# Kernel tuning notes

Measured on AMD Instinct MI355X. Metric: run time of the kernel, lower is better.

The kernel has to match this reference:

```python
import jax, jax.numpy as jnp
import numpy as np

HID, FFN, NE, TOPK = 1024, 4096, 8, 2


def setup_inputs() -> dict:
    key = jax.random.key(0)
    ks = jax.random.split(key, 4)
    x = jax.random.normal(ks[0], (2, 2048, HID), dtype=jnp.float32)
    # router: nn.Linear(hidden, num_experts, bias=False), init std=0.02; stored as [H, E]
    Wr = jax.random.normal(ks[1], (HID, NE), dtype=jnp.float32) * 0.02
    # per-expert FFN weights stacked on leading expert axis
    W1 = jax.random.normal(ks[2], (NE, HID, FFN), dtype=jnp.float32) * (1.0 / np.sqrt(HID))
    b1 = jnp.zeros((NE, FFN), dtype=jnp.float32)
    W2 = jax.random.normal(ks[3], (NE, FFN, HID), dtype=jnp.float32) * (1.0 / np.sqrt(FFN))
    b2 = jnp.zeros((NE, HID), dtype=jnp.float32)
    return {"x": x, "Wr": Wr, "W1": W1, "b1": b1, "W2": W2, "b2": b2}


def reference(x, Wr, W1, b1, W2, b2):
    B, S, H = x.shape
    E = Wr.shape[1]
    T = B * S
    xf = x.reshape(T, H)                                  # [T, H]
    logits = xf @ Wr                                      # [T, E]
    probs = jax.nn.softmax(logits, axis=-1)
    topk_p, topk_i = jax.lax.top_k(probs, TOPK)           # [T, K]
    topk_p = topk_p / jnp.sum(topk_p, axis=-1, keepdims=True)
    # dense combine weights: c[t, e] = normalized prob if expert e selected for token t else 0
    c = jnp.zeros((T, E), dtype=xf.dtype).at[jnp.arange(T)[:, None], topk_i].add(topk_p)

    def expert_step(acc, ew):
        w1, bb1, w2, bb2, ce = ew                         # ce: [T]
        h = jax.nn.gelu(xf @ w1 + bb1, approximate=False)  # exact GELU like nn.GELU()
        y = h @ w2 + bb2                                  # [T, H]
        return acc + ce[:, None] * y, None

    out, _ = jax.lax.scan(expert_step, jnp.zeros_like(xf), (W1, b1, W2, b2, c.T))
    return out.reshape(B, S, H)
```

## Files before the change

### kernel.cpp

```cpp
#include <hip/hip_runtime.h>
#include <hip/hip_bf16.h>

#define H 1024
#define F 4096
#define NE 8
#define T 4096

typedef unsigned short u16;
typedef float floatx4 __attribute__((ext_vector_type(4)));
typedef short short8 __attribute__((ext_vector_type(8)));

__device__ __forceinline__ u16 f2bf(float f) {
  union { float f; unsigned int u; } c; c.f = f;
  unsigned int u = c.u;
  return (u16)((u + 0x7fffu + ((u >> 16) & 1u)) >> 16);
}

__device__ __forceinline__ void load16_lds(const u16* g, u16* l) {
  __builtin_amdgcn_global_load_lds(
      (const __attribute__((address_space(1))) unsigned int*)g,
      (__attribute__((address_space(3))) unsigned int*)l, 16, 0, 0);
}

__device__ __forceinline__ float gelu_f(float v) {
  float y = fabsf(v) * 0.70710678118f;
  float t = __builtin_amdgcn_rcpf(fmaf(0.3275911f, y, 1.0f));
  float p = t * fmaf(t, fmaf(t, fmaf(t, fmaf(t, 1.061405429f, -1.453152027f),
                                     1.421413741f), -0.284496736f), 0.254829592f);
  float e = __builtin_amdgcn_exp2f(-y * y * 1.44269504f);
  float erfv = fmaf(-p, e, 1.0f);
  return fmaf(0.5f * fabsf(v), erfv, 0.5f * v);
}

__global__ __launch_bounds__(256) void router_kernel(
    const float* __restrict__ x, const float* __restrict__ Wr,
    int* __restrict__ cnt, int* __restrict__ tok, float* __restrict__ wgt) {
  int t = (blockIdx.x * 256 + threadIdx.x) >> 6;
  int lane = threadIdx.x & 63;
  const float* xr = x + (size_t)t * H;
  double p[NE];
#pragma unroll
  for (int e = 0; e < NE; ++e) p[e] = 0.0;
  for (int k = lane; k < H; k += 64) {
    float xv = xr[k];
    const float4* wr4 = reinterpret_cast<const float4*>(Wr + k * NE);
    float4 a = wr4[0], b = wr4[1];
    p[0] += (double)xv * a.x; p[1] += (double)xv * a.y;
    p[2] += (double)xv * a.z; p[3] += (double)xv * a.w;
    p[4] += (double)xv * b.x; p[5] += (double)xv * b.y;
    p[6] += (double)xv * b.z; p[7] += (double)xv * b.w;
  }
#pragma unroll
  for (int e = 0; e < NE; ++e) {
#pragma unroll
    for (int off = 32; off; off >>= 1) p[e] += __shfl_down(p[e], off, 64);
  }
  if (lane == 0) {
    int i0 = 0;
#pragma unroll
    for (int e = 1; e < NE; ++e) if (p[e] > p[i0]) i0 = e;
    int i1 = (i0 == 0) ? 1 : 0;
#pragma unroll
    for (int e = 0; e < NE; ++e) if (e != i0 && p[e] > p[i1]) i1 = e;
    double d = exp(p[i1] - p[i0]);
    float w0 = (float)(1.0 / (1.0 + d));
    float w1 = (float)(d / (1.0 + d));
    int pos0 = atomicAdd(&cnt[i0], 1);
    tok[i0 * T + pos0] = t;
    wgt[i0 * T + pos0] = w0;
    int pos1 = atomicAdd(&cnt[i1], 1);
    tok[i1 * T + pos1] = t | 4096;
    wgt[i1 * T + pos1] = w1;
  }
}

__global__ void offsets_kernel(const int* __restrict__ cnt, int* __restrict__ off) {
  if (threadIdx.x == 0) {
    int s = 0;
#pragma unroll
    for (int e = 0; e < NE; ++e) { off[e] = s; s += cnt[e]; }
    off[NE] = s;
  }
}

__global__ __launch_bounds__(256) void convert_x_kernel(
    const float* __restrict__ x, u16* __restrict__ xb) {
  int i = blockIdx.x * 256 + threadIdx.x;
  float4 v = reinterpret_cast<const float4*>(x)[i];
  ushort4 o;
  o.x = f2bf(v.x); o.y = f2bf(v.y); o.z = f2bf(v.z); o.w = f2bf(v.w);
  reinterpret_cast<ushort4*>(xb)[i] = o;
}

__global__ __launch_bounds__(256) void transpose_both_kernel(
    const float* __restrict__ W1, const float* __restrict__ W2,
    u16* __restrict__ W1t, u16* __restrict__ W2t) {
  __shared__ u16 tile[64][76];
  int z = blockIdx.z;
  int e = z & 7;
  const float* s; u16* d; int R, C, c0, r0;
  if (z < NE) {
    s = W1 + (size_t)e * H * F; d = W1t + (size_t)e * H * F;
    R = H; C = F; c0 = blockIdx.x << 6; r0 = blockIdx.y << 6;
  } else {
    s = W2 + (size_t)e * F * H; d = W2t + (size_t)e * F * H;
    R = F; C = H; c0 = blockIdx.y << 6; r0 = blockIdx.x << 6;
  }
  int t = threadIdx.x;
  int rl = t >> 4, cl = (t & 15) << 2;
#pragma unroll
  for (int i = 0; i < 4; ++i) {
    float4 v = *reinterpret_cast<const float4*>(&s[(size_t)(r0 + rl + i * 16) * C + c0 + cl]);
    ushort4 o; o.x = f2bf(v.x); o.y = f2bf(v.y); o.z = f2bf(v.z); o.w = f2bf(v.w);
    *reinterpret_cast<ushort4*>(&tile[rl + i * 16][cl]) = o;
  }
  __syncthreads();
  int cw = t >> 3, rw = (t & 7) << 3;
#pragma unroll
  for (int i = 0; i < 2; ++i) {
    int c = cw + i * 32;
    short8 o;
#pragma unroll
    for (int j = 0; j < 8; ++j) o[j] = (short)tile[rw + j][c];
    *reinterpret_cast<short8*>(&d[(size_t)(c0 + c) * R + r0 + rw]) = o;
  }
}

__global__ __launch_bounds__(256) void gemm1_kernel(
    const u16* __restrict__ Xb, const u16* __restrict__ W1t,
    const float* __restrict__ b1, const int* __restrict__ cnt,
    const int* __restrict__ off, const int* __restrict__ tok,
    u16* __restrict__ Hc) {
  int e = blockIdx.z;
  int n = cnt[e];
  int m0 = blockIdx.y << 7;
  if (m0 >= n) return;
  int n0 = blockIdx.x << 7;
  int rb = off[e];

  __shared__ alignas(16) u16 As[2][128 * 32];
  __shared__ alignas(16) u16 Bs[2][128 * 32];
  __shared__ int tokS[128];

  int tid = threadIdx.x;
  if (tid < 128) {
    int s = m0 + tid;
    tokS[tid] = (s < n) ? (tok[e * T + s] & 4095) : 0;
  }
  __syncthreads();

  int kchunk = (((tid & 3) ^ ((tid >> 3) & 3))) * 8;
  const u16* W1e = W1t + (size_t)e * F * H;
  const u16* aP0 = Xb + (size_t)tokS[tid >> 2] * H + kchunk;
  const u16* aP1 = Xb + (size_t)tokS[64 + (tid >> 2)] * H + kchunk;
  const u16* bP0 = W1e + (size_t)(n0 + (tid >> 2)) * H + kchunk;
  const u16* bP1 = W1e + (size_t)(n0 + 64 + (tid >> 2)) * H + kchunk;

  int wv = tid >> 6, lane = tid & 63;
  int wm = wv >> 1, wn = wv & 1;
  int quad = lane >> 4, l16 = lane & 15;

  floatx4 acc[4][4];
#pragma unroll
  for (int mt = 0; mt < 4; ++mt)
#pragma unroll
    for (int nt = 0; nt < 4; ++nt) acc[mt][nt] = floatx4{0.f, 0.f, 0.f, 0.f};

  int qa = (quad ^ ((l16 >> 1) & 3)) * 8;
  int aOff[4], bOff[4];
#pragma unroll
  for (int i = 0; i < 4; ++i) {
    aOff[i] = (wm * 64 + i * 16 + l16) * 32 + qa;
    bOff[i] = (wn * 64 + i * 16 + l16) * 32 + qa;
  }

#define STAGE1(buf, kk)                                   \
  do {                                                    \
    load16_lds(aP0 + (kk), &As[buf][tid * 8]);            \
    load16_lds(aP1 + (kk), &As[buf][(tid + 256) * 8]);    \
    load16_lds(bP0 + (kk), &Bs[buf][tid * 8]);            \
    load16_lds(bP1 + (kk), &Bs[buf][(tid + 256) * 8]);    \
  } while (0)

  const int NIT = H / 32;
  STAGE1(0, 0);
  STAGE1(1, 32);
  for (int it = 0; it < NIT; ++it) {
    if (it >= NIT - 1) asm volatile("s_waitcnt vmcnt(0)" ::: "memory");
    else               asm volatile("s_waitcnt vmcnt(4)" ::: "memory");
    __builtin_amdgcn_s_barrier();
    int cur = it & 1;
    short8 av[4], bv[4];
#pragma unroll
    for (int i = 0; i < 4; ++i) {
      av[i] = *reinterpret_cast<const short8*>(&As[cur][aOff[i]]);
      bv[i] = *reinterpret_cast<const short8*>(&Bs[cur][bOff[i]]);
    }
#pragma unroll
    for (int mt = 0; mt < 4; ++mt)
#pragma unroll
      for (int nt = 0; nt < 4; ++nt)
        acc[mt][nt] = __builtin_amdgcn_mfma_f32_16x16x32_bf16(av[mt], bv[nt], acc[mt][nt], 0, 0, 0);
    __builtin_amdgcn_s_barrier();
    if (it + 2 < NIT) STAGE1(cur, (it + 2) * 32);
  }
#undef STAGE1

  float b1v[4];
#pragma unroll
  for (int nt = 0; nt < 4; ++nt)
    b1v[nt] = b1[e * F + n0 + wn * 64 + nt * 16 + l16];
#pragma unroll
  for (int mt = 0; mt < 4; ++mt) {
#pragma unroll
    for (int i = 0; i < 4; ++i) {
      int row = wm * 64 + mt * 16 + quad * 4 + i;
      int gr = m0 + row;
      if (gr < n) {
        u16* hrow = Hc + (size_t)(rb + gr) * F + n0 + wn * 64 + l16;
#pragma unroll
        for (int nt = 0; nt < 4; ++nt) {
          float v = acc[mt][nt][i] + b1v[nt];
          hrow[nt * 16] = f2bf(gelu_f(v));
        }
      }
    }
  }
}

__global__ __launch_bounds__(256) void gemm2_kernel(
    const u16* __restrict__ Hc, const u16* __restrict__ W2t,
    const float* __restrict__ b2, const int* __restrict__ cnt,
    const int* __restrict__ off, const int* __restrict__ tok,
    const float* __restrict__ wgt, float* __restrict__ Yb) {
  int bid = blockIdx.x;
  int e = bid & 7;
  int rem = bid >> 3;
  int by = rem & 31;
  int bx = rem >> 5;
  int n = cnt[e];
  int m0 = by << 7;
  if (m0 >= n) return;
  int n0 = bx << 7;
  int rb = off[e];

  __shared__ alignas(16) u16 As[2][128 * 32];
  __shared__ alignas(16) u16 Bs[2][128 * 32];

  int tid = threadIdx.x;
  int kchunk = (((tid & 3) ^ ((tid >> 3) & 3))) * 8;
  const u16* W2e = W2t + (size_t)e * F * H;
  const u16* aP0 = Hc + (size_t)(rb + m0 + (tid >> 2)) * F + kchunk;
  const u16* aP1 = Hc + (size_t)(rb + m0 + 64 + (tid >> 2)) * F + kchunk;
  const u16* bP0 = W2e + (size_t)(n0 + (tid >> 2)) * F + kchunk;
  const u16* bP1 = W2e + (size_t)(n0 + 64 + (tid >> 2)) * F + kchunk;

  int wv = tid >> 6, lane = tid & 63;
  int wm = wv >> 1, wn = wv & 1;
  int quad = lane >> 4, l16 = lane & 15;

  floatx4 acc[4][4];
#pragma unroll
  for (int mt = 0; mt < 4; ++mt)
#pragma unroll
    for (int nt = 0; nt < 4; ++nt) acc[mt][nt] = floatx4{0.f, 0.f, 0.f, 0.f};

  int qa = (quad ^ ((l16 >> 1) & 3)) * 8;
  int aOff[4], bOff[4];
#pragma unroll
  for (int i = 0; i < 4; ++i) {
    aOff[i] = (wm * 64 + i * 16 + l16) * 32 + qa;
    bOff[i] = (wn * 64 + i * 16 + l16) * 32 + qa;
  }

#define STAGE2(buf, kk)                                   \
  do {                                                    \
    load16_lds(aP0 + (kk), &As[buf][tid * 8]);            \
    load16_lds(aP1 + (kk), &As[buf][(tid + 256) * 8]);    \
    load16_lds(bP0 + (kk), &Bs[buf][tid * 8]);            \
    load16_lds(bP1 + (kk), &Bs[buf][(tid + 256) * 8]);    \
  } while (0)

  const int NIT = F / 32;
  STAGE2(0, 0);
  STAGE2(1, 32);
  for (int it = 0; it < NIT; ++it) {
    if (it >= NIT - 1) asm volatile("s_waitcnt vmcnt(0)" ::: "memory");
    else               asm volatile("s_waitcnt vmcnt(4)" ::: "memory");
    __builtin_amdgcn_s_barrier();
    int cur = it & 1;
    short8 av[4], bv[4];
#pragma unroll
    for (int i = 0; i < 4; ++i) {
      av[i] = *reinterpret_cast<const short8*>(&As[cur][aOff[i]]);
      bv[i] = *reinterpret_cast<const short8*>(&Bs[cur][bOff[i]]);
    }
#pragma unroll
    for (int mt = 0; mt < 4; ++mt)
#pragma unroll
      for (int nt = 0; nt < 4; ++nt)
        acc[mt][nt] = __builtin_amdgcn_mfma_f32_16x16x32_bf16(av[mt], bv[nt], acc[mt][nt], 0, 0, 0);
    __builtin_amdgcn_s_barrier();
    if (it + 2 < NIT) STAGE2(cur, (it + 2) * 32);
  }
#undef STAGE2

  float b2v[4];
#pragma unroll
  for (int nt = 0; nt < 4; ++nt)
    b2v[nt] = b2[e * H + n0 + wn * 64 + nt * 16 + l16];
#pragma unroll
  for (int mt = 0; mt < 4; ++mt) {
#pragma unroll
    for (int i = 0; i < 4; ++i) {
      int row = wm * 64 + mt * 16 + quad * 4 + i;
      int gr = m0 + row;
      if (gr < n) {
        float wv2 = wgt[e * T + gr];
        int tk = tok[e * T + gr];
        int t2 = tk & 4095, slot = tk >> 12;
        float* yrow = Yb + ((size_t)t2 * 2 + slot) * H + n0 + wn * 64 + l16;
#pragma unroll
        for (int nt = 0; nt < 4; ++nt)
          yrow[nt * 16] = (acc[mt][nt][i] + b2v[nt]) * wv2;
      }
    }
  }
}

__global__ __launch_bounds__(256) void combine_kernel(
    const float* __restrict__ Yb, float* __restrict__ out) {
  int i = blockIdx.x * 256 + threadIdx.x;
  int t = i >> 8;
  int h4 = i & 255;
  const float4* Y4 = reinterpret_cast<const float4*>(Yb);
  float4 a = Y4[((size_t)t * 2) * 256 + h4];
  float4 b = Y4[((size_t)t * 2 + 1) * 256 + h4];
  float4 o; o.x = a.x + b.x; o.y = a.y + b.y; o.z = a.z + b.z; o.w = a.w + b.w;
  reinterpret_cast<float4*>(out)[i] = o;
}

extern "C" void kernel_launch(void* const* d_in, const int* in_sizes, int n_in,
                              void* d_out, int out_size, void* d_ws, size_t ws_size,
                              hipStream_t stream) {
  const float* x  = (const float*)d_in[0];
  const float* Wr = (const float*)d_in[1];
  const float* W1 = (const float*)d_in[2];
  const float* b1 = (const float*)d_in[3];
  const float* W2 = (const float*)d_in[4];
  const float* b2 = (const float*)d_in[5];
  float* out = (float*)d_out;

  char* ws = (char*)d_ws;
  int*   cnt = (int*)(ws + 0);
  int*   off = (int*)(ws + 256);
  int*   tok = (int*)(ws + 4096);
  float* wgt = (float*)(ws + 135168);
  u16*   Xb  = (u16*)(ws + 266240);
  u16*   W1t = (u16*)(ws + 8654848);
  u16*   W2t = (u16*)(ws + 75763712);
  u16*   Hc  = (u16*)(ws + 142872576);
  float* Yb  = (float*)(ws + 8654848);

  hipMemsetAsync(cnt, 0, 64, stream);

  router_kernel<<<dim3(T / 4), dim3(256), 0, stream>>>(x, Wr, cnt, tok, wgt);
  offsets_kernel<<<dim3(1), dim3(64), 0, stream>>>(cnt, off);
  convert_x_kernel<<<dim3((T * H / 4) / 256), dim3(256), 0, stream>>>(x, Xb);
  transpose_both_kernel<<<dim3(64, 16, 16), dim3(256), 0, stream>>>(W1, W2, W1t, W2t);
  gemm1_kernel<<<dim3(F / 128, 32, NE), dim3(256), 0, stream>>>(Xb, W1t, b1, cnt, off, tok, Hc);
  gemm2_kernel<<<dim3(2048), dim3(256), 0, stream>>>(Hc, W2t, b2, cnt, off, tok, wgt, Yb);
  combine_kernel<<<dim3(T * H / 4 / 256), dim3(256), 0, stream>>>(Yb, out);
}
```

Measured before the change: 666.1 us.

## Fuse prep kernels into one launch and switch GEMMs to 2-wave blocks

```diff
diff --git a/kernel.cpp b/kernel.cpp
--- a/kernel.cpp
+++ b/kernel.cpp
@@ -32,82 +32,75 @@
   return fmaf(0.5f * fabsf(v), erfv, 0.5f * v);
 }
 
-__global__ __launch_bounds__(256) void router_kernel(
+__global__ __launch_bounds__(256) void prep_kernel(
     const float* __restrict__ x, const float* __restrict__ Wr,
-    int* __restrict__ cnt, int* __restrict__ tok, float* __restrict__ wgt) {
-  int t = (blockIdx.x * 256 + threadIdx.x) >> 6;
-  int lane = threadIdx.x & 63;
-  const float* xr = x + (size_t)t * H;
-  double p[NE];
-#pragma unroll
-  for (int e = 0; e < NE; ++e) p[e] = 0.0;
-  for (int k = lane; k < H; k += 64) {
-    float xv = xr[k];
-    const float4* wr4 = reinterpret_cast<const float4*>(Wr + k * NE);
-    float4 a = wr4[0], b = wr4[1];
-    p[0] += (double)xv * a.x; p[1] += (double)xv * a.y;
-    p[2] += (double)xv * a.z; p[3] += (double)xv * a.w;
-    p[4] += (double)xv * b.x; p[5] += (double)xv * b.y;
-    p[6] += (double)xv * b.z; p[7] += (double)xv * b.w;
-  }
-#pragma unroll
-  for (int e = 0; e < NE; ++e) {
-#pragma unroll
-    for (int off = 32; off; off >>= 1) p[e] += __shfl_down(p[e], off, 64);
-  }
-  if (lane == 0) {
-    int i0 = 0;
-#pragma unroll
-    for (int e = 1; e < NE; ++e) if (p[e] > p[i0]) i0 = e;
-    int i1 = (i0 == 0) ? 1 : 0;
-#pragma unroll
-    for (int e = 0; e < NE; ++e) if (e != i0 && p[e] > p[i1]) i1 = e;
-    double d = exp(p[i1] - p[i0]);
-    float w0 = (float)(1.0 / (1.0 + d));
-    float w1 = (float)(d / (1.0 + d));
-    int pos0 = atomicAdd(&cnt[i0], 1);
-    tok[i0 * T + pos0] = t;
-    wgt[i0 * T + pos0] = w0;
-    int pos1 = atomicAdd(&cnt[i1], 1);
-    tok[i1 * T + pos1] = t | 4096;
-    wgt[i1 * T + pos1] = w1;
-  }
-}
-
-__global__ void offsets_kernel(const int* __restrict__ cnt, int* __restrict__ off) {
-  if (threadIdx.x == 0) {
-    int s = 0;
-#pragma unroll
-    for (int e = 0; e < NE; ++e) { off[e] = s; s += cnt[e]; }
-    off[NE] = s;
-  }
-}
-
-__global__ __launch_bounds__(256) void convert_x_kernel(
-    const float* __restrict__ x, u16* __restrict__ xb) {
-  int i = blockIdx.x * 256 + threadIdx.x;
-  float4 v = reinterpret_cast<const float4*>(x)[i];
-  ushort4 o;
-  o.x = f2bf(v.x); o.y = f2bf(v.y); o.z = f2bf(v.z); o.w = f2bf(v.w);
-  reinterpret_cast<ushort4*>(xb)[i] = o;
-}
-
-__global__ __launch_bounds__(256) void transpose_both_kernel(
     const float* __restrict__ W1, const float* __restrict__ W2,
-    u16* __restrict__ W1t, u16* __restrict__ W2t) {
+    int* __restrict__ cnt, int* __restrict__ tok, float* __restrict__ wgt,
+    u16* __restrict__ xb, u16* __restrict__ W1t, u16* __restrict__ W2t) {
   __shared__ u16 tile[64][76];
-  int z = blockIdx.z;
-  int e = z & 7;
+  int bid = blockIdx.x;
+  int tid = threadIdx.x;
+  if (bid < 1024) {
+    int t = (bid * 256 + tid) >> 6;
+    int lane = tid & 63;
+    const float* xr = x + (size_t)t * H;
+    double p[NE];
+#pragma unroll
+    for (int e = 0; e < NE; ++e) p[e] = 0.0;
+    for (int k = lane; k < H; k += 64) {
+      float xv = xr[k];
+      const float4* wr4 = reinterpret_cast<const float4*>(Wr + k * NE);
+      float4 a = wr4[0], b = wr4[1];
+      p[0] += (double)xv * a.x; p[1] += (double)xv * a.y;
+      p[2] += (double)xv * a.z; p[3] += (double)xv * a.w;
+      p[4] += (double)xv * b.x; p[5] += (double)xv * b.y;
+      p[6] += (double)xv * b.z; p[7] += (double)xv * b.w;
+    }
+#pragma unroll
+    for (int e = 0; e < NE; ++e) {
+#pragma unroll
+      for (int off = 32; off; off >>= 1) p[e] += __shfl_down(p[e], off, 64);
+    }
+    if (lane == 0) {
+      int i0 = 0;
+#pragma unroll
+      for (int e = 1; e < NE; ++e) if (p[e] > p[i0]) i0 = e;
+      int i1 = (i0 == 0) ? 1 : 0;
+#pragma unroll
+      for (int e = 0; e < NE; ++e) if (e != i0 && p[e] > p[i1]) i1 = e;
+      double d = exp(p[i1] - p[i0]);
+      float w0 = (float)(1.0 / (1.0 + d));
+      float w1 = (float)(d / (1.0 + d));
+      int pos0 = atomicAdd(&cnt[i0], 1);
+      tok[i0 * T + pos0] = t;
+      wgt[i0 * T + pos0] = w0;
+      int pos1 = atomicAdd(&cnt[i1], 1);
+      tok[i1 * T + pos1] = t | 4096;
+      wgt[i1 * T + pos1] = w1;
+    }
+    return;
+  }
+  if (bid < 5120) {
+    int i = (bid - 1024) * 256 + tid;
+    float4 v = reinterpret_cast<const float4*>(x)[i];
+    ushort4 o;
+    o.x = f2bf(v.x); o.y = f2bf(v.y); o.z = f2bf(v.z); o.w = f2bf(v.w);
+    reinterpret_cast<ushort4*>(xb)[i] = o;
+    return;
+  }
+  int b = bid - 5120;
   const float* s; u16* d; int R, C, c0, r0;
-  if (z < NE) {
+  if (b < 8192) {
+    int e = b >> 10, rem = b & 1023;
     s = W1 + (size_t)e * H * F; d = W1t + (size_t)e * H * F;
-    R = H; C = F; c0 = blockIdx.x << 6; r0 = blockIdx.y << 6;
+    R = H; C = F; c0 = (rem & 63) << 6; r0 = (rem >> 6) << 6;
   } else {
+    int b2 = b - 8192;
+    int e = b2 >> 10, rem = b2 & 1023;
     s = W2 + (size_t)e * F * H; d = W2t + (size_t)e * F * H;
-    R = F; C = H; c0 = blockIdx.y << 6; r0 = blockIdx.x << 6;
-  }
-  int t = threadIdx.x;
-  int rl = t >> 4, cl = (t & 15) << 2;
+    R = F; C = H; r0 = (rem & 63) << 6; c0 = (rem >> 6) << 6;
+  }
+  int rl = tid >> 4, cl = (tid & 15) << 2;
 #pragma unroll
   for (int i = 0; i < 4; ++i) {
     float4 v = *reinterpret_cast<const float4*>(&s[(size_t)(r0 + rl + i * 16) * C + c0 + cl]);
@@ -115,7 +108,7 @@
     *reinterpret_cast<ushort4*>(&tile[rl + i * 16][cl]) = o;
   }
   __syncthreads();
-  int cw = t >> 3, rw = (t & 7) << 3;
+  int cw = tid >> 3, rw = (tid & 7) << 3;
 #pragma unroll
   for (int i = 0; i < 2; ++i) {
     int c = cw + i * 32;
@@ -126,7 +119,17 @@
   }
 }
 
-__global__ __launch_bounds__(256) void gemm1_kernel(
+__global__ void offsets_kernel(const int* __restrict__ cnt, int* __restrict__ off) {
+  if (threadIdx.x == 0) {
+    int s = 0;
+#pragma unroll
+    for (int e = 0; e < NE; ++e) { off[e] = s; s += cnt[e]; }
+    off[NE] = s;
+  }
+}
+
+
+__global__ __launch_bounds__(128, 2) void gemm1_kernel(
     const u16* __restrict__ Xb, const u16* __restrict__ W1t,
     const float* __restrict__ b1, const int* __restrict__ cnt,
     const int* __restrict__ off, const int* __restrict__ tok,
@@ -143,43 +146,46 @@
   __shared__ int tokS[128];
 
   int tid = threadIdx.x;
-  if (tid < 128) {
+  {
     int s = m0 + tid;
     tokS[tid] = (s < n) ? (tok[e * T + s] & 4095) : 0;
   }
   __syncthreads();
 
-  int kchunk = (((tid & 3) ^ ((tid >> 3) & 3))) * 8;
   const u16* W1e = W1t + (size_t)e * F * H;
-  const u16* aP0 = Xb + (size_t)tokS[tid >> 2] * H + kchunk;
-  const u16* aP1 = Xb + (size_t)tokS[64 + (tid >> 2)] * H + kchunk;
-  const u16* bP0 = W1e + (size_t)(n0 + (tid >> 2)) * H + kchunk;
-  const u16* bP1 = W1e + (size_t)(n0 + 64 + (tid >> 2)) * H + kchunk;
+  const u16* aP[4]; const u16* bP[4];
+#pragma unroll
+  for (int s = 0; s < 4; ++s) {
+    int c = tid + s * 128;
+    int r = c >> 2, p = c & 3;
+    int kcc = (p ^ ((r >> 1) & 3)) * 8;
+    aP[s] = Xb + (size_t)tokS[r] * H + kcc;
+    bP[s] = W1e + (size_t)(n0 + r) * H + kcc;
+  }
 
   int wv = tid >> 6, lane = tid & 63;
-  int wm = wv >> 1, wn = wv & 1;
   int quad = lane >> 4, l16 = lane & 15;
 
-  floatx4 acc[4][4];
+  floatx4 acc[4][8];
 #pragma unroll
   for (int mt = 0; mt < 4; ++mt)
 #pragma unroll
-    for (int nt = 0; nt < 4; ++nt) acc[mt][nt] = floatx4{0.f, 0.f, 0.f, 0.f};
+    for (int nt = 0; nt < 8; ++nt) acc[mt][nt] = floatx4{0.f, 0.f, 0.f, 0.f};
 
   int qa = (quad ^ ((l16 >> 1) & 3)) * 8;
-  int aOff[4], bOff[4];
-#pragma unroll
-  for (int i = 0; i < 4; ++i) {
-    aOff[i] = (wm * 64 + i * 16 + l16) * 32 + qa;
-    bOff[i] = (wn * 64 + i * 16 + l16) * 32 + qa;
-  }
-
-#define STAGE1(buf, kk)                                   \
-  do {                                                    \
-    load16_lds(aP0 + (kk), &As[buf][tid * 8]);            \
-    load16_lds(aP1 + (kk), &As[buf][(tid + 256) * 8]);    \
-    load16_lds(bP0 + (kk), &Bs[buf][tid * 8]);            \
-    load16_lds(bP1 + (kk), &Bs[buf][(tid + 256) * 8]);    \
+  int aOff[4], bOff[8];
+#pragma unroll
+  for (int i = 0; i < 4; ++i) aOff[i] = (wv * 64 + i * 16 + l16) * 32 + qa;
+#pragma unroll
+  for (int i = 0; i < 8; ++i) bOff[i] = (i * 16 + l16) * 32 + qa;
+
+#define STAGE1(buf, kk)                                              \
+  do {                                                               \
+    _Pragma("unroll")                                                \
+    for (int s = 0; s < 4; ++s) {                                    \
+      load16_lds(aP[s] + (kk), &As[buf][(tid + s * 128) * 8]);       \
+      load16_lds(bP[s] + (kk), &Bs[buf][(tid + s * 128) * 8]);       \
+    }                                                                \
   } while (0)
 
   const int NIT = H / 32;
@@ -187,39 +193,39 @@
   STAGE1(1, 32);
   for (int it = 0; it < NIT; ++it) {
     if (it >= NIT - 1) asm volatile("s_waitcnt vmcnt(0)" ::: "memory");
-    else               asm volatile("s_waitcnt vmcnt(4)" ::: "memory");
+    else               asm volatile("s_waitcnt vmcnt(8)" ::: "memory");
     __builtin_amdgcn_s_barrier();
     int cur = it & 1;
-    short8 av[4], bv[4];
-#pragma unroll
-    for (int i = 0; i < 4; ++i) {
-      av[i] = *reinterpret_cast<const short8*>(&As[cur][aOff[i]]);
+    short8 bv[8];
+#pragma unroll
+    for (int i = 0; i < 8; ++i)
       bv[i] = *reinterpret_cast<const short8*>(&Bs[cur][bOff[i]]);
-    }
-#pragma unroll
-    for (int mt = 0; mt < 4; ++mt)
-#pragma unroll
-      for (int nt = 0; nt < 4; ++nt)
-        acc[mt][nt] = __builtin_amdgcn_mfma_f32_16x16x32_bf16(av[mt], bv[nt], acc[mt][nt], 0, 0, 0);
+#pragma unroll
+    for (int mt = 0; mt < 4; ++mt) {
+      short8 av = *reinterpret_cast<const short8*>(&As[cur][aOff[mt]]);
+#pragma unroll
+      for (int nt = 0; nt < 8; ++nt)
+        acc[mt][nt] = __builtin_amdgcn_mfma_f32_16x16x32_bf16(av, bv[nt], acc[mt][nt], 0, 0, 0);
+    }
     __builtin_amdgcn_s_barrier();
     if (it + 2 < NIT) STAGE1(cur, (it + 2) * 32);
   }
 #undef STAGE1
 
-  float b1v[4];
-#pragma unroll
-  for (int nt = 0; nt < 4; ++nt)
-    b1v[nt] = b1[e * F + n0 + wn * 64 + nt * 16 + l16];
+  float b1v[8];
+#pragma unroll
+  for (int nt = 0; nt < 8; ++nt)
+    b1v[nt] = b1[e * F + n0 + nt * 16 + l16];
 #pragma unroll
   for (int mt = 0; mt < 4; ++mt) {
 #pragma unroll
     for (int i = 0; i < 4; ++i) {
-      int row = wm * 64 + mt * 16 + quad * 4 + i;
+      int row = wv * 64 + mt * 16 + quad * 4 + i;
       int gr = m0 + row;
       if (gr < n) {
-        u16* hrow = Hc + (size_t)(rb + gr) * F + n0 + wn * 64 + l16;
-#pragma unroll
-        for (int nt = 0; nt < 4; ++nt) {
+        u16* hrow = Hc + (size_t)(rb + gr) * F + n0 + l16;
+#pragma unroll
+        for (int nt = 0; nt < 8; ++nt) {
           float v = acc[mt][nt][i] + b1v[nt];
           hrow[nt * 16] = f2bf(gelu_f(v));
         }
@@ -228,7 +234,7 @@
   }
 }
 
-__global__ __launch_bounds__(256) void gemm2_kernel(
+__global__ __launch_bounds__(128, 2) void gemm2_kernel(
     const u16* __restrict__ Hc, const u16* __restrict__ W2t,
     const float* __restrict__ b2, const int* __restrict__ cnt,
     const int* __restrict__ off, const int* __restrict__ tok,
@@ -248,37 +254,40 @@
   __shared__ alignas(16) u16 Bs[2][128 * 32];
 
   int tid = threadIdx.x;
-  int kchunk = (((tid & 3) ^ ((tid >> 3) & 3))) * 8;
   const u16* W2e = W2t + (size_t)e * F * H;
-  const u16* aP0 = Hc + (size_t)(rb + m0 + (tid >> 2)) * F + kchunk;
-  const u16* aP1 = Hc + (size_t)(rb + m0 + 64 + (tid >> 2)) * F + kchunk;
-  const u16* bP0 = W2e + (size_t)(n0 + (tid >> 2)) * F + kchunk;
-  const u16* bP1 = W2e + (size_t)(n0 + 64 + (tid >> 2)) * F + kchunk;
+  const u16* aP[4]; const u16* bP[4];
+#pragma unroll
+  for (int s = 0; s < 4; ++s) {
+    int c = tid + s * 128;
+    int r = c >> 2, p = c & 3;
+    int kcc = (p ^ ((r >> 1) & 3)) * 8;
+    aP[s] = Hc + (size_t)(rb + m0 + r) * F + kcc;
+    bP[s] = W2e + (size_t)(n0 + r) * F + kcc;
+  }
 
   int wv = tid >> 6, lane = tid & 63;
-  int wm = wv >> 1, wn = wv & 1;
   int quad = lane >> 4, l16 = lane & 15;
 
-  floatx4 acc[4][4];
+  floatx4 acc[4][8];
 #pragma unroll
   for (int mt = 0; mt < 4; ++mt)
 #pragma unroll
-    for (int nt = 0; nt < 4; ++nt) acc[mt][nt] = floatx4{0.f, 0.f, 0.f, 0.f};
+    for (int nt = 0; nt < 8; ++nt) acc[mt][nt] = floatx4{0.f, 0.f, 0.f, 0.f};
 
   int qa = (quad ^ ((l16 >> 1) & 3)) * 8;
-  int aOff[4], bOff[4];
-#pragma unroll
-  for (int i = 0; i < 4; ++i) {
-    aOff[i] = (wm * 64 + i * 16 + l16) * 32 + qa;
-    bOff[i] = (wn * 64 + i * 16 + l16) * 32 + qa;
-  }
-
-#define STAGE2(buf, kk)                                   \
-  do {                                                    \
-    load16_lds(aP0 + (kk), &As[buf][tid * 8]);            \
-    load16_lds(aP1 + (kk), &As[buf][(tid + 256) * 8]);    \
-    load16_lds(bP0 + (kk), &Bs[buf][tid * 8]);            \
-    load16_lds(bP1 + (kk), &Bs[buf][(tid + 256) * 8]);    \
+  int aOff[4], bOff[8];
+#pragma unroll
+  for (int i = 0; i < 4; ++i) aOff[i] = (wv * 64 + i * 16 + l16) * 32 + qa;
+#pragma unroll
+  for (int i = 0; i < 8; ++i) bOff[i] = (i * 16 + l16) * 32 + qa;
+
+#define STAGE2(buf, kk)                                              \
+  do {                                                               \
+    _Pragma("unroll")                                                \
+    for (int s = 0; s < 4; ++s) {                                    \
+      load16_lds(aP[s] + (kk), &As[buf][(tid + s * 128) * 8]);       \
+      load16_lds(bP[s] + (kk), &Bs[buf][(tid + s * 128) * 8]);       \
+    }                                                                \
   } while (0)
 
   const int NIT = F / 32;
@@ -286,42 +295,42 @@
   STAGE2(1, 32);
   for (int it = 0; it < NIT; ++it) {
     if (it >= NIT - 1) asm volatile("s_waitcnt vmcnt(0)" ::: "memory");
-    else               asm volatile("s_waitcnt vmcnt(4)" ::: "memory");
+    else               asm volatile("s_waitcnt vmcnt(8)" ::: "memory");
     __builtin_amdgcn_s_barrier();
     int cur = it & 1;
-    short8 av[4], bv[4];
-#pragma unroll
-    for (int i = 0; i < 4; ++i) {
-      av[i] = *reinterpret_cast<const short8*>(&As[cur][aOff[i]]);
+    short8 bv[8];
+#pragma unroll
+    for (int i = 0; i < 8; ++i)
       bv[i] = *reinterpret_cast<const short8*>(&Bs[cur][bOff[i]]);
-    }
-#pragma unroll
-    for (int mt = 0; mt < 4; ++mt)
-#pragma unroll
-      for (int nt = 0; nt < 4; ++nt)
-        acc[mt][nt] = __builtin_amdgcn_mfma_f32_16x16x32_bf16(av[mt], bv[nt], acc[mt][nt], 0, 0, 0);
+#pragma unroll
+    for (int mt = 0; mt < 4; ++mt) {
+      short8 av = *reinterpret_cast<const short8*>(&As[cur][aOff[mt]]);
+#pragma unroll
+      for (int nt = 0; nt < 8; ++nt)
+        acc[mt][nt] = __builtin_amdgcn_mfma_f32_16x16x32_bf16(av, bv[nt], acc[mt][nt], 0, 0, 0);
+    }
     __builtin_amdgcn_s_barrier();
     if (it + 2 < NIT) STAGE2(cur, (it + 2) * 32);
   }
 #undef STAGE2
 
-  float b2v[4];
-#pragma unroll
-  for (int nt = 0; nt < 4; ++nt)
-    b2v[nt] = b2[e * H + n0 + wn * 64 + nt * 16 + l16];
+  float b2v[8];
+#pragma unroll
+  for (int nt = 0; nt < 8; ++nt)
+    b2v[nt] = b2[e * H + n0 + nt * 16 + l16];
 #pragma unroll
   for (int mt = 0; mt < 4; ++mt) {
 #pragma unroll
     for (int i = 0; i < 4; ++i) {
-      int row = wm * 64 + mt * 16 + quad * 4 + i;
+      int row = wv * 64 + mt * 16 + quad * 4 + i;
       int gr = m0 + row;
       if (gr < n) {
         float wv2 = wgt[e * T + gr];
         int tk = tok[e * T + gr];
         int t2 = tk & 4095, slot = tk >> 12;
-        float* yrow = Yb + ((size_t)t2 * 2 + slot) * H + n0 + wn * 64 + l16;
-#pragma unroll
-        for (int nt = 0; nt < 4; ++nt)
+        float* yrow = Yb + ((size_t)t2 * 2 + slot) * H + n0 + l16;
+#pragma unroll
+        for (int nt = 0; nt < 8; ++nt)
           yrow[nt * 16] = (acc[mt][nt][i] + b2v[nt]) * wv2;
       }
     }
@@ -364,11 +373,9 @@
 
   hipMemsetAsync(cnt, 0, 64, stream);
 
-  router_kernel<<<dim3(T / 4), dim3(256), 0, stream>>>(x, Wr, cnt, tok, wgt);
+  prep_kernel<<<dim3(21504), dim3(256), 0, stream>>>(x, Wr, W1, W2, cnt, tok, wgt, Xb, W1t, W2t);
   offsets_kernel<<<dim3(1), dim3(64), 0, stream>>>(cnt, off);
-  convert_x_kernel<<<dim3((T * H / 4) / 256), dim3(256), 0, stream>>>(x, Xb);
-  transpose_both_kernel<<<dim3(64, 16, 16), dim3(256), 0, stream>>>(W1, W2, W1t, W2t);
-  gemm1_kernel<<<dim3(F / 128, 32, NE), dim3(256), 0, stream>>>(Xb, W1t, b1, cnt, off, tok, Hc);
-  gemm2_kernel<<<dim3(2048), dim3(256), 0, stream>>>(Hc, W2t, b2, cnt, off, tok, wgt, Yb);
+  gemm1_kernel<<<dim3(F / 128, 32, NE), dim3(128), 0, stream>>>(Xb, W1t, b1, cnt, off, tok, Hc);
+  gemm2_kernel<<<dim3(2048), dim3(128), 0, stream>>>(Hc, W2t, b2, cnt, off, tok, wgt, Yb);
   combine_kernel<<<dim3(T * H / 4 / 256), dim3(256), 0, stream>>>(Yb, out);
 }
```

Result: no change. 665.7 us (-0.1%).
